# Optimization experiments

Measured on AMD Instinct MI355X. Metric: run time of the kernel, lower is better.

Reference implementation:

```python
import jax, jax.numpy as jnp
import numpy as np

B, T, F, H = 64, 512, 128, 512
NUM_LAYERS = 3


def _lstm_layer(x_tbf, W_ih, W_hh, b_ih, b_hh):
    # x_tbf: [T, B, in], W_ih: [4H, in], W_hh: [4H, H]
    # PyTorch gate order: i, f, g, o
    Hd = W_hh.shape[1]
    Bd = x_tbf.shape[1]
    # precompute input projections for all timesteps (one big GEMM)
    x_proj = jnp.einsum('tbf,gf->tbg', x_tbf, W_ih) + b_ih  # [T, B, 4H]

    def step(carry, xp_t):
        h, c = carry
        gates = xp_t + h @ W_hh.T + b_hh  # [B, 4H]
        i, f, g, o = jnp.split(gates, 4, axis=-1)
        i = jax.nn.sigmoid(i)
        f = jax.nn.sigmoid(f)
        g = jnp.tanh(g)
        o = jax.nn.sigmoid(o)
        c = f * c + i * g
        h = o * jnp.tanh(c)
        return (h, c), h

    h0 = jnp.zeros((Bd, Hd), x_tbf.dtype)
    c0 = jnp.zeros((Bd, Hd), x_tbf.dtype)
    _, hs = jax.lax.scan(step, (h0, c0), x_proj)
    return hs  # [T, B, H]


def setup_inputs() -> dict:
    key = jax.random.key(0)
    ks = jax.random.split(key, 20)
    s = 1.0 / np.sqrt(H)
    inp = {"input_tensor": jax.random.normal(ks[0], (B, T, F), jnp.float32)}
    in_dims = [F, H, H]
    ki = 1
    for l in range(NUM_LAYERS):
        inp[f"W_ih{l}"] = jax.random.uniform(ks[ki], (4 * H, in_dims[l]), jnp.float32, -s, s); ki += 1
        inp[f"W_hh{l}"] = jax.random.uniform(ks[ki], (4 * H, H), jnp.float32, -s, s); ki += 1
        inp[f"b_ih{l}"] = jax.random.uniform(ks[ki], (4 * H,), jnp.float32, -s, s); ki += 1
        inp[f"b_hh{l}"] = jax.random.uniform(ks[ki], (4 * H,), jnp.float32, -s, s); ki += 1
    s1 = 1.0 / np.sqrt(H)
    inp["fc_W1"] = jax.random.uniform(ks[13], (64, H), jnp.float32, -s1, s1)
    inp["fc_b1"] = jax.random.uniform(ks[14], (64,), jnp.float32, -s1, s1)
    s2 = 1.0 / np.sqrt(64)
    inp["fc_W2"] = jax.random.uniform(ks[15], (1, 64), jnp.float32, -s2, s2)
    inp["fc_b2"] = jax.random.uniform(ks[16], (1,), jnp.float32, -s2, s2)
    return inp


def reference(input_tensor, W_ih0, W_hh0, b_ih0, b_hh0,
              W_ih1, W_hh1, b_ih1, b_hh1,
              W_ih2, W_hh2, b_ih2, b_hh2,
              fc_W1, fc_b1, fc_W2, fc_b2):
    x = jnp.transpose(input_tensor, (1, 0, 2))  # [T, B, F]
    x = _lstm_layer(x, W_ih0, W_hh0, b_ih0, b_hh0)
    x = _lstm_layer(x, W_ih1, W_hh1, b_ih1, b_hh1)  # eval mode: no dropout
    x = _lstm_layer(x, W_ih2, W_hh2, b_ih2, b_hh2)
    last = x[-1]  # [B, H]
    h1 = jax.nn.relu(last @ fc_W1.T + fc_b1)
    out = jax.nn.relu(h1 @ fc_W2.T + fc_b2)  # [B, 1]
    return out
```

## Files before the change

### kernel.cpp

```cpp
#include <hip/hip_runtime.h>
#include <hip/hip_fp16.h>
#include <math.h>

#define B_ 64
#define T_ 512
#define F_ 128
#define H_ 512
#define NBLK 96
#define SPIN_MAX (1 << 20)

typedef _Float16 f16x8 __attribute__((ext_vector_type(8)));
typedef float f32x4 __attribute__((ext_vector_type(4)));
typedef int   i32x4 __attribute__((ext_vector_type(4)));

__device__ __forceinline__ unsigned short f2h(float f) {
    return __half_as_ushort(__float2half(f));
}
__device__ __forceinline__ float h2f(unsigned short u) {
    return __half2float(__ushort_as_half(u));
}

__global__ void transpose_x(const float* __restrict__ in, unsigned* __restrict__ xs) {
    const int t = blockIdx.x;
    for (int idx = threadIdx.x; idx < B_ * F_ / 4; idx += blockDim.x) {
        const int kp2 = idx >> 6;
        const int bb = idx & 63;
        const float* src = in + (size_t)bb * T_ * F_ + (size_t)t * F_ + 4 * kp2;
        const unsigned h0 = f2h(src[0]), h1 = f2h(src[1]);
        const unsigned h2 = f2h(src[2]), h3 = f2h(src[3]);
        const unsigned dw0 = h0 | (h1 << 16);
        const unsigned dw1 = h2 | (h3 << 16);
        *(unsigned long long*)(xs + (size_t)t * 4096 + (size_t)kp2 * 128 + bb * 2) =
            ((unsigned long long)dw1 << 32) | dw0;
    }
}

__device__ __forceinline__ float sigmoid_(float x) {
    return __builtin_amdgcn_rcpf(1.0f + __expf(-x));
}
__device__ __forceinline__ float tanh_(float x) {
    return 1.0f - 2.0f * __builtin_amdgcn_rcpf(1.0f + __expf(2.0f * x));
}

__device__ __forceinline__ unsigned long long loadc_u64(const unsigned* p) {
    return __hip_atomic_load((const unsigned long long*)p, __ATOMIC_RELAXED,
                             __HIP_MEMORY_SCOPE_AGENT);
}
__device__ __forceinline__ unsigned loadc_u32(const unsigned* p) {
    return __hip_atomic_load(p, __ATOMIC_RELAXED, __HIP_MEMORY_SCOPE_AGENT);
}
__device__ __forceinline__ void storec_u64(unsigned* p, unsigned long long v) {
    __hip_atomic_store((unsigned long long*)p, v, __ATOMIC_RELAXED,
                       __HIP_MEMORY_SCOPE_AGENT);
}
__device__ __forceinline__ void storec_f(float* p, float v) {
    __hip_atomic_store(p, v, __ATOMIC_RELAXED, __HIP_MEMORY_SCOPE_AGENT);
}
__device__ __forceinline__ float loadc_f(const float* p) {
    return __hip_atomic_load(p, __ATOMIC_RELAXED, __HIP_MEMORY_SCOPE_AGENT);
}
__device__ __forceinline__ int loadc_i(const int* p) {
    return __hip_atomic_load(p, __ATOMIC_RELAXED, __HIP_MEMORY_SCOPE_AGENT);
}
__device__ __forceinline__ void storec_i(int* p, int v) {
    __hip_atomic_store(p, v, __ATOMIC_RELAXED, __HIP_MEMORY_SCOPE_AGENT);
}

__device__ __forceinline__ void gbar_arrive(int* __restrict__ slots, int bid,
                                            int tid, int e) {
    asm volatile("s_waitcnt vmcnt(0) lgkmcnt(0)" ::: "memory");
    __syncthreads();
    if (tid == 0) storec_i(&slots[bid * 16], e);
}
__device__ __forceinline__ void gbar_wait(const int* __restrict__ slots, int tid,
                                          int e) {
    if (tid < NBLK) {
        int g = 0;
        while (loadc_i(&slots[tid * 16]) < e && ++g < SPIN_MAX)
            __builtin_amdgcn_s_sleep(1);
    }
    __syncthreads();
}

template <int NKX, bool XPLAIN>
__device__ void scan_layer(const unsigned* __restrict__ xb,
                           unsigned* __restrict__ hbuf,
                           int* __restrict__ slots, int bid, int tid,
                           const unsigned short* __restrict__ wfrag,
                           const float (&bias)[4][4], const int (&hstore)[4],
                           int lane, int q, int laneoff, int twol) {
    float c_reg[4] = {0.f, 0.f, 0.f, 0.f};
    unsigned long long vx[NKX][2];
    union Frag { i32x4 i4; f16x8 s; };

    auto pref = [&](int tt) {
        if (tt < 0 || tt >= T_) return;
        const unsigned* xsrc = XPLAIN ? (xb + (size_t)tt * 4096 + laneoff)
                                      : (xb + (size_t)(tt & 3) * 16384 + laneoff);
#pragma unroll
        for (int i = 0; i < NKX; ++i) {
            if (XPLAIN) {
                vx[i][0] = *(const unsigned long long*)(xsrc + i * 1024);
                vx[i][1] = *(const unsigned long long*)(xsrc + i * 1024 + 128);
            } else {
                vx[i][0] = loadc_u64(xsrc + i * 1024);
                vx[i][1] = loadc_u64(xsrc + i * 1024 + 128);
            }
        }
    };

    if (XPLAIN) pref(0);

    for (int s = 0; s < T_ + 4; ++s) {
        const int t = s - twol;
        if (t >= 0 && t < T_) {
            unsigned long long vh[16][2];
            const unsigned* hs = hbuf + (size_t)((t + 3) & 3) * 16384 + laneoff;
#pragma unroll
            for (int j = 0; j < 16; ++j) {
                vh[j][0] = loadc_u64(hs + j * 1024);
                vh[j][1] = loadc_u64(hs + j * 1024 + 128);
            }

            f32x4 acc[4] = {{0.f,0.f,0.f,0.f},{0.f,0.f,0.f,0.f},
                            {0.f,0.f,0.f,0.f},{0.f,0.f,0.f,0.f}};
#pragma unroll
            for (int i = 0; i < NKX; ++i) {
                Frag Bf, A0, A1, A2, A3;
                Bf.i4[0] = (int)(unsigned)vx[i][0];
                Bf.i4[1] = (int)(unsigned)(vx[i][0] >> 32);
                Bf.i4[2] = (int)(unsigned)vx[i][1];
                Bf.i4[3] = (int)(unsigned)(vx[i][1] >> 32);
                A0.i4 = *(const i32x4*)&wfrag[i * 2048 + lane * 8];
                A1.i4 = *(const i32x4*)&wfrag[i * 2048 + 512 + lane * 8];
                A2.i4 = *(const i32x4*)&wfrag[i * 2048 + 1024 + lane * 8];
                A3.i4 = *(const i32x4*)&wfrag[i * 2048 + 1536 + lane * 8];
                acc[0] = __builtin_amdgcn_mfma_f32_16x16x32_f16(A0.s, Bf.s, acc[0], 0, 0, 0);
                acc[1] = __builtin_amdgcn_mfma_f32_16x16x32_f16(A1.s, Bf.s, acc[1], 0, 0, 0);
                acc[2] = __builtin_amdgcn_mfma_f32_16x16x32_f16(A2.s, Bf.s, acc[2], 0, 0, 0);
                acc[3] = __builtin_amdgcn_mfma_f32_16x16x32_f16(A3.s, Bf.s, acc[3], 0, 0, 0);
            }
#pragma unroll
            for (int j = 0; j < 16; ++j) {
                Frag Bf, A0, A1, A2, A3;
                Bf.i4[0] = (int)(unsigned)vh[j][0];
                Bf.i4[1] = (int)(unsigned)(vh[j][0] >> 32);
                Bf.i4[2] = (int)(unsigned)vh[j][1];
                Bf.i4[3] = (int)(unsigned)(vh[j][1] >> 32);
                const int i = NKX + j;
                A0.i4 = *(const i32x4*)&wfrag[i * 2048 + lane * 8];
                A1.i4 = *(const i32x4*)&wfrag[i * 2048 + 512 + lane * 8];
                A2.i4 = *(const i32x4*)&wfrag[i * 2048 + 1024 + lane * 8];
                A3.i4 = *(const i32x4*)&wfrag[i * 2048 + 1536 + lane * 8];
                acc[0] = __builtin_amdgcn_mfma_f32_16x16x32_f16(A0.s, Bf.s, acc[0], 0, 0, 0);
                acc[1] = __builtin_amdgcn_mfma_f32_16x16x32_f16(A1.s, Bf.s, acc[1], 0, 0, 0);
                acc[2] = __builtin_amdgcn_mfma_f32_16x16x32_f16(A2.s, Bf.s, acc[2], 0, 0, 0);
                acc[3] = __builtin_amdgcn_mfma_f32_16x16x32_f16(A3.s, Bf.s, acc[3], 0, 0, 0);
            }

#pragma unroll
            for (int rg = 0; rg < 4; ++rg) {
                float a[4];
#pragma unroll
                for (int g = 0; g < 4; ++g) a[g] = bias[rg][g] + acc[rg][g];
                const float ig = sigmoid_(a[0]);
                const float fg = sigmoid_(a[1]);
                const float gg = tanh_(a[2]);
                const float og = sigmoid_(a[3]);
                c_reg[rg] = fg * c_reg[rg] + ig * gg;
                const float hv = og * tanh_(c_reg[rg]);
                const unsigned P0 = (unsigned)f2h(hv);
                const unsigned P1 = (unsigned)__shfl_xor((int)P0, 16, 64) & 0xFFFFu;
                const unsigned D  = P0 | (P1 << 16);
                const unsigned D2 = (unsigned)__shfl_xor((int)D, 32, 64);
                if (q == 0)
                    storec_u64(hbuf + (size_t)(t & 3) * 16384 + hstore[rg],
                               ((unsigned long long)D2 << 32) | D);
            }
        }
        gbar_arrive(slots, bid, tid, s + 1);
        __builtin_amdgcn_sched_barrier(0);
        pref(s + 1 - twol);
        __builtin_amdgcn_sched_barrier(0);
        gbar_wait(slots, tid, s + 1);
    }
}

__global__ void __launch_bounds__(256, 1) lstm_scan(
    const unsigned* __restrict__ xs, unsigned* __restrict__ hbf,
    float* __restrict__ h1s, float* __restrict__ out,
    int* __restrict__ bar_slots,
    const float* __restrict__ Wih0, const float* __restrict__ Whh0,
    const float* __restrict__ bih0, const float* __restrict__ bhh0,
    const float* __restrict__ Wih1, const float* __restrict__ Whh1,
    const float* __restrict__ bih1, const float* __restrict__ bhh1,
    const float* __restrict__ Wih2, const float* __restrict__ Whh2,
    const float* __restrict__ bih2, const float* __restrict__ bhh2,
    const float* __restrict__ fcW1, const float* __restrict__ fcb1,
    const float* __restrict__ fcW2, const float* __restrict__ fcb2) {
    __shared__ unsigned short wfrag[32 * 2048];
    __shared__ float redsc[4 * 64];

    const float* WihA[3] = {Wih0, Wih1, Wih2};
    const float* WhhA[3] = {Whh0, Whh1, Whh2};
    const float* bihA[3] = {bih0, bih1, bih2};
    const float* bhhA[3] = {bhh0, bhh1, bhh2};

    const int tid   = threadIdx.x;
    const int bid   = blockIdx.x;
    const int layer = bid >> 5;
    const int cb    = bid & 31;
    const int c0    = cb * 16;
    const int lane  = tid & 63;
    const int w     = __builtin_amdgcn_readfirstlane(tid >> 6);
    const int KX    = (layer == 0) ? F_ : H_;
    const int NK    = KX / 32 + 16;

    const float* wih = WihA[layer];
    const float* whh = WhhA[layer];

    for (int idx = tid; idx < NK * 2048; idx += 256) {
        const int i = idx >> 11, rem = idx & 2047;
        const int rg = rem >> 9, r2 = rem & 511;
        const int l = r2 >> 3, j = r2 & 7;
        const int m = l & 15;
        const int grow = (m & 3) * 512 + c0 + rg * 4 + (m >> 2);
        const int k = i * 32 + (l >> 4) * 8 + j;
        const float f = (k < KX) ? wih[(size_t)grow * KX + k]
                                 : whh[(size_t)grow * 512 + (k - KX)];
        wfrag[i * 2048 + rg * 512 + l * 8 + j] = f2h(f);
    }
    __syncthreads();

    const int fb = w * 16 + (lane & 15);
    const int q  = lane >> 4;
    float bias[4][4];
#pragma unroll
    for (int rg = 0; rg < 4; ++rg)
#pragma unroll
        for (int g = 0; g < 4; ++g)
            bias[rg][g] = bihA[layer][g * 512 + c0 + rg * 4 + q] +
                          bhhA[layer][g * 512 + c0 + rg * 4 + q];

    int hstore[4];
#pragma unroll
    for (int rg = 0; rg < 4; ++rg) hstore[rg] = (cb * 4 + rg) * 128 + fb * 2;
    const int laneoff = q * 256 + fb * 2;

    unsigned* hbuf = hbf + (size_t)layer * 4 * 16384;
    const unsigned* xb =
        (layer == 0) ? xs : (hbf + (size_t)(layer - 1) * 4 * 16384);

    if (layer == 0)
        scan_layer<4, true>(xb, hbuf, bar_slots, bid, tid, wfrag, bias, hstore,
                            lane, q, laneoff, 0);
    else if (layer == 1)
        scan_layer<16, false>(xb, hbuf, bar_slots, bid, tid, wfrag, bias,
                              hstore, lane, q, laneoff, 2);
    else
        scan_layer<16, false>(xb, hbuf, bar_slots, bid, tid, wfrag, bias,
                              hstore, lane, q, laneoff, 4);

    const unsigned* h2u = hbf + (size_t)2 * 4 * 16384 + (size_t)3 * 16384;
    const int fcb = tid & 63;
    if (bid < 64) {
        float part = 0.0f;
        const float* wrow = fcW1 + (size_t)bid * H_ + w * 128;
#pragma unroll 8
        for (int k = 0; k < 128; ++k) {
            const int kk = w * 128 + k;
            const unsigned dv =
                loadc_u32(h2u + (kk >> 2) * 128 + fcb * 2 + ((kk >> 1) & 1));
            const float val = h2f((unsigned short)((dv >> ((kk & 1) * 16)) & 0xFFFFu));
            part = fmaf(wrow[k], val, part);
        }
        redsc[w * 64 + fcb] = part;
        __syncthreads();
        if (tid < 64) {
            float acc2 = fcb1[bid] + redsc[tid] + redsc[64 + tid] +
                         redsc[128 + tid] + redsc[192 + tid];
            storec_f(&h1s[bid * B_ + tid], fmaxf(acc2, 0.0f));
        }
    }
    gbar_arrive(bar_slots, bid, tid, T_ + 5);
    gbar_wait(bar_slots, tid, T_ + 5);
    if (bid == 0 && tid < 64) {
        float acc2 = fcb2[0];
#pragma unroll
        for (int c = 0; c < 64; ++c)
            acc2 = fmaf(fcW2[c], loadc_f(&h1s[c * B_ + tid]), acc2);
        out[tid] = fmaxf(acc2, 0.0f);
    }
}

extern "C" void kernel_launch(void* const* d_in, const int* in_sizes, int n_in,
                              void* d_out, int out_size, void* d_ws, size_t ws_size,
                              hipStream_t stream) {
    const float* in    = (const float*)d_in[0];
    const float* Wih0  = (const float*)d_in[1];
    const float* Whh0  = (const float*)d_in[2];
    const float* bih0  = (const float*)d_in[3];
    const float* bhh0  = (const float*)d_in[4];
    const float* Wih1  = (const float*)d_in[5];
    const float* Whh1  = (const float*)d_in[6];
    const float* bih1  = (const float*)d_in[7];
    const float* bhh1  = (const float*)d_in[8];
    const float* Wih2  = (const float*)d_in[9];
    const float* Whh2  = (const float*)d_in[10];
    const float* bih2  = (const float*)d_in[11];
    const float* bhh2  = (const float*)d_in[12];
    const float* fcW1  = (const float*)d_in[13];
    const float* fcb1  = (const float*)d_in[14];
    const float* fcW2  = (const float*)d_in[15];
    const float* fcb2  = (const float*)d_in[16];
    float* outp = (float*)d_out;

    unsigned* xs  = (unsigned*)d_ws;
    unsigned* hbf = xs + (size_t)T_ * 4096;
    float* h1s = (float*)(hbf + (size_t)3 * 4 * 16384);
    int* bar_slots = (int*)(h1s + 64 * 64);

    hipMemsetAsync(hbf, 0,
                   ((size_t)3 * 4 * 16384 + 64 * 64 + NBLK * 16 + 16) * sizeof(int),
                   stream);

    transpose_x<<<dim3(T_), dim3(256), 0, stream>>>(in, xs);

    void* args[] = {
        (void*)&xs, (void*)&hbf, (void*)&h1s, (void*)&outp, (void*)&bar_slots,
        (void*)&Wih0, (void*)&Whh0, (void*)&bih0, (void*)&bhh0,
        (void*)&Wih1, (void*)&Whh1, (void*)&bih1, (void*)&bhh1,
        (void*)&Wih2, (void*)&Whh2, (void*)&bih2, (void*)&bhh2,
        (void*)&fcW1, (void*)&fcb1, (void*)&fcW2, (void*)&fcb2};
    hipLaunchCooperativeKernel((void*)lstm_scan, dim3(NBLK), dim3(256), args, 0, stream);
}
```

Baseline: 2.721 ms.

## Tag hidden-state entries with timestep to drop memory drain from grid barrier

Each stored hidden-state half-pair now carries its timestep tag in the upper 32 bits. Consumers re-read until all tags match, which lets the per-step grid barrier skip the s_waitcnt drain. The inter-layer skew is cut from 2 to 1 step, so the scan needs fewer total steps, and the FC head validates the final layer's tags before reading. This doubles the hidden-buffer traffic and adds spin-retry loads. Correctness now rests on 64-bit relaxed atomics being seen whole, and the retry loop gives up after a fixed bound.

```diff
diff --git a/kernel.cpp b/kernel.cpp
--- a/kernel.cpp
+++ b/kernel.cpp
@@ -8,6 +8,7 @@
 #define H_ 512
 #define NBLK 96
 #define SPIN_MAX (1 << 20)
+#define GUARD_RETRY 4096
 
 typedef _Float16 f16x8 __attribute__((ext_vector_type(8)));
 typedef float f32x4 __attribute__((ext_vector_type(4)));
@@ -46,9 +47,6 @@
     return __hip_atomic_load((const unsigned long long*)p, __ATOMIC_RELAXED,
                              __HIP_MEMORY_SCOPE_AGENT);
 }
-__device__ __forceinline__ unsigned loadc_u32(const unsigned* p) {
-    return __hip_atomic_load(p, __ATOMIC_RELAXED, __HIP_MEMORY_SCOPE_AGENT);
-}
 __device__ __forceinline__ void storec_u64(unsigned* p, unsigned long long v) {
     __hip_atomic_store((unsigned long long*)p, v, __ATOMIC_RELAXED,
                        __HIP_MEMORY_SCOPE_AGENT);
@@ -66,14 +64,10 @@
     __hip_atomic_store(p, v, __ATOMIC_RELAXED, __HIP_MEMORY_SCOPE_AGENT);
 }
 
-__device__ __forceinline__ void gbar_arrive(int* __restrict__ slots, int bid,
-                                            int tid, int e) {
-    asm volatile("s_waitcnt vmcnt(0) lgkmcnt(0)" ::: "memory");
+__device__ __forceinline__ void gbar_nd(int* __restrict__ slots, int bid,
+                                        int tid, int e) {
     __syncthreads();
     if (tid == 0) storec_i(&slots[bid * 16], e);
-}
-__device__ __forceinline__ void gbar_wait(const int* __restrict__ slots, int tid,
-                                          int e) {
     if (tid < NBLK) {
         int g = 0;
         while (loadc_i(&slots[tid * 16]) < e && ++g < SPIN_MAX)
@@ -81,45 +75,95 @@
     }
     __syncthreads();
 }
-
-template <int NKX, bool XPLAIN>
+__device__ __forceinline__ void gbar_drain(int* __restrict__ slots, int bid,
+                                           int tid, int e) {
+    asm volatile("s_waitcnt vmcnt(0) lgkmcnt(0)" ::: "memory");
+    __syncthreads();
+    if (tid == 0) storec_i(&slots[bid * 16], e);
+    if (tid < NBLK) {
+        int g = 0;
+        while (loadc_i(&slots[tid * 16]) < e && ++g < SPIN_MAX)
+            __builtin_amdgcn_s_sleep(1);
+    }
+    __syncthreads();
+}
+
+template <int NKX, bool XTAG>
 __device__ void scan_layer(const unsigned* __restrict__ xb,
                            unsigned* __restrict__ hbuf,
                            int* __restrict__ slots, int bid, int tid,
                            const unsigned short* __restrict__ wfrag,
-                           const float (&bias)[4][4], const int (&hstore)[4],
-                           int lane, int q, int laneoff, int twol) {
+                           const float (&bias)[4][4], int lane, int q, int fb,
+                           int cb, int layer) {
+    union Frag { i32x4 i4; f16x8 s; };
     float c_reg[4] = {0.f, 0.f, 0.f, 0.f};
-    unsigned long long vx[NKX][2];
-    union Frag { i32x4 i4; f16x8 s; };
-
-    auto pref = [&](int tt) {
-        if (tt < 0 || tt >= T_) return;
-        const unsigned* xsrc = XPLAIN ? (xb + (size_t)tt * 4096 + laneoff)
-                                      : (xb + (size_t)(tt & 3) * 16384 + laneoff);
-#pragma unroll
-        for (int i = 0; i < NKX; ++i) {
-            if (XPLAIN) {
-                vx[i][0] = *(const unsigned long long*)(xsrc + i * 1024);
-                vx[i][1] = *(const unsigned long long*)(xsrc + i * 1024 + 128);
-            } else {
-                vx[i][0] = loadc_u64(xsrc + i * 1024);
-                vx[i][1] = loadc_u64(xsrc + i * 1024 + 128);
-            }
-        }
-    };
-
-    if (XPLAIN) pref(0);
-
-    for (int s = 0; s < T_ + 4; ++s) {
-        const int t = s - twol;
+    const int ho = fb * 4;
+    const int xo_plain = q * 256 + fb * 2;
+    int hstE[4];
+#pragma unroll
+    for (int rg = 0; rg < 4; ++rg) hstE[rg] = (cb * 4 + rg) * 256 + fb * 4;
+
+    for (int s = 0; s < T_ + 2; ++s) {
+        const int t = s - layer;
         if (t >= 0 && t < T_) {
-            unsigned long long vh[16][2];
-            const unsigned* hs = hbuf + (size_t)((t + 3) & 3) * 16384 + laneoff;
-#pragma unroll
-            for (int j = 0; j < 16; ++j) {
-                vh[j][0] = loadc_u64(hs + j * 1024);
-                vh[j][1] = loadc_u64(hs + j * 1024 + 128);
+            unsigned long long vh[32][2];
+            unsigned long long vx[XTAG ? 32 : NKX][2];
+
+            const unsigned* hsl = hbuf + (size_t)((t + 3) & 3) * 32768 + ho;
+            const unsigned* xsl = XTAG ? (xb + (size_t)(t & 3) * 32768 + ho)
+                                       : (xb + (size_t)t * 4096 + xo_plain);
+
+            auto issue_x = [&]() {
+                if constexpr (XTAG) {
+#pragma unroll
+                    for (int i = 0; i < 16; ++i) {
+                        const unsigned* e0 = xsl + (8 * i + 2 * q) * 256;
+                        vx[2 * i][0]     = loadc_u64(e0);
+                        vx[2 * i][1]     = loadc_u64(e0 + 2);
+                        vx[2 * i + 1][0] = loadc_u64(e0 + 256);
+                        vx[2 * i + 1][1] = loadc_u64(e0 + 258);
+                    }
+                } else {
+#pragma unroll
+                    for (int i = 0; i < NKX; ++i) {
+                        vx[i][0] = *(const unsigned long long*)(xsl + i * 1024);
+                        vx[i][1] = *(const unsigned long long*)(xsl + i * 1024 + 128);
+                    }
+                }
+            };
+            auto issue_h = [&]() {
+#pragma unroll
+                for (int j = 0; j < 16; ++j) {
+                    const unsigned* e0 = hsl + (8 * j + 2 * q) * 256;
+                    vh[2 * j][0]     = loadc_u64(e0);
+                    vh[2 * j][1]     = loadc_u64(e0 + 2);
+                    vh[2 * j + 1][0] = loadc_u64(e0 + 256);
+                    vh[2 * j + 1][1] = loadc_u64(e0 + 258);
+                }
+            };
+
+            issue_x();
+            issue_h();
+
+            const unsigned htag = (unsigned)t;
+            const unsigned xtag = (unsigned)(t + 1);
+            int guard = 0;
+            for (;;) {
+                int ok = 1;
+#pragma unroll
+                for (int e = 0; e < 32; ++e)
+                    ok &= ((unsigned)(vh[e][0] >> 32) == htag) &
+                          ((unsigned)(vh[e][1] >> 32) == htag);
+                if constexpr (XTAG) {
+#pragma unroll
+                    for (int e = 0; e < 32; ++e)
+                        ok &= ((unsigned)(vx[e][0] >> 32) == xtag) &
+                              ((unsigned)(vx[e][1] >> 32) == xtag);
+                }
+                if (__all(ok)) break;
+                if (++guard > GUARD_RETRY) break;
+                issue_x();
+                issue_h();
             }
 
             f32x4 acc[4] = {{0.f,0.f,0.f,0.f},{0.f,0.f,0.f,0.f},
@@ -127,10 +171,17 @@
 #pragma unroll
             for (int i = 0; i < NKX; ++i) {
                 Frag Bf, A0, A1, A2, A3;
-                Bf.i4[0] = (int)(unsigned)vx[i][0];
-                Bf.i4[1] = (int)(unsigned)(vx[i][0] >> 32);
-                Bf.i4[2] = (int)(unsigned)vx[i][1];
-                Bf.i4[3] = (int)(unsigned)(vx[i][1] >> 32);
+                if constexpr (XTAG) {
+                    Bf.i4[0] = (int)(unsigned)vx[2 * i][0];
+                    Bf.i4[1] = (int)(unsigned)vx[2 * i][1];
+                    Bf.i4[2] = (int)(unsigned)vx[2 * i + 1][0];
+                    Bf.i4[3] = (int)(unsigned)vx[2 * i + 1][1];
+                } else {
+                    Bf.i4[0] = (int)(unsigned)vx[i][0];
+                    Bf.i4[1] = (int)(unsigned)(vx[i][0] >> 32);
+                    Bf.i4[2] = (int)(unsigned)vx[i][1];
+                    Bf.i4[3] = (int)(unsigned)(vx[i][1] >> 32);
+                }
                 A0.i4 = *(const i32x4*)&wfrag[i * 2048 + lane * 8];
                 A1.i4 = *(const i32x4*)&wfrag[i * 2048 + 512 + lane * 8];
                 A2.i4 = *(const i32x4*)&wfrag[i * 2048 + 1024 + lane * 8];
@@ -143,10 +194,10 @@
 #pragma unroll
             for (int j = 0; j < 16; ++j) {
                 Frag Bf, A0, A1, A2, A3;
-                Bf.i4[0] = (int)(unsigned)vh[j][0];
-                Bf.i4[1] = (int)(unsigned)(vh[j][0] >> 32);
-                Bf.i4[2] = (int)(unsigned)vh[j][1];
-                Bf.i4[3] = (int)(unsigned)(vh[j][1] >> 32);
+                Bf.i4[0] = (int)(unsigned)vh[2 * j][0];
+                Bf.i4[1] = (int)(unsigned)vh[2 * j][1];
+                Bf.i4[2] = (int)(unsigned)vh[2 * j + 1][0];
+                Bf.i4[3] = (int)(unsigned)vh[2 * j + 1][1];
                 const int i = NKX + j;
                 A0.i4 = *(const i32x4*)&wfrag[i * 2048 + lane * 8];
                 A1.i4 = *(const i32x4*)&wfrag[i * 2048 + 512 + lane * 8];
@@ -173,16 +224,15 @@
                 const unsigned P1 = (unsigned)__shfl_xor((int)P0, 16, 64) & 0xFFFFu;
                 const unsigned D  = P0 | (P1 << 16);
                 const unsigned D2 = (unsigned)__shfl_xor((int)D, 32, 64);
-                if (q == 0)
-                    storec_u64(hbuf + (size_t)(t & 3) * 16384 + hstore[rg],
-                               ((unsigned long long)D2 << 32) | D);
+                if (q == 0) {
+                    unsigned* eb = hbuf + (size_t)(t & 3) * 32768 + hstE[rg];
+                    const unsigned long long tg = (unsigned long long)(t + 1) << 32;
+                    storec_u64(eb, tg | D);
+                    storec_u64(eb + 2, tg | D2);
+                }
             }
         }
-        gbar_arrive(slots, bid, tid, s + 1);
-        __builtin_amdgcn_sched_barrier(0);
-        pref(s + 1 - twol);
-        __builtin_amdgcn_sched_barrier(0);
-        gbar_wait(slots, tid, s + 1);
+        gbar_nd(slots, bid, tid, s + 1);
     }
 }
 
@@ -242,37 +292,49 @@
             bias[rg][g] = bihA[layer][g * 512 + c0 + rg * 4 + q] +
                           bhhA[layer][g * 512 + c0 + rg * 4 + q];
 
-    int hstore[4];
-#pragma unroll
-    for (int rg = 0; rg < 4; ++rg) hstore[rg] = (cb * 4 + rg) * 128 + fb * 2;
-    const int laneoff = q * 256 + fb * 2;
-
-    unsigned* hbuf = hbf + (size_t)layer * 4 * 16384;
+    unsigned* hbuf = hbf + (size_t)layer * 4 * 32768;
     const unsigned* xb =
-        (layer == 0) ? xs : (hbf + (size_t)(layer - 1) * 4 * 16384);
+        (layer == 0) ? xs : (hbf + (size_t)(layer - 1) * 4 * 32768);
 
     if (layer == 0)
-        scan_layer<4, true>(xb, hbuf, bar_slots, bid, tid, wfrag, bias, hstore,
-                            lane, q, laneoff, 0);
+        scan_layer<4, false>(xb, hbuf, bar_slots, bid, tid, wfrag, bias, lane,
+                             q, fb, cb, 0);
     else if (layer == 1)
-        scan_layer<16, false>(xb, hbuf, bar_slots, bid, tid, wfrag, bias,
-                              hstore, lane, q, laneoff, 2);
+        scan_layer<16, true>(xb, hbuf, bar_slots, bid, tid, wfrag, bias, lane,
+                             q, fb, cb, 1);
     else
-        scan_layer<16, false>(xb, hbuf, bar_slots, bid, tid, wfrag, bias,
-                              hstore, lane, q, laneoff, 4);
-
-    const unsigned* h2u = hbf + (size_t)2 * 4 * 16384 + (size_t)3 * 16384;
+        scan_layer<16, true>(xb, hbuf, bar_slots, bid, tid, wfrag, bias, lane,
+                             q, fb, cb, 2);
+
     const int fcb = tid & 63;
     if (bid < 64) {
+        const unsigned* h2b = hbf + (size_t)2 * 4 * 32768 + (size_t)3 * 32768;
+        unsigned long long ef[32][2];
+        int guard = 0;
+        for (;;) {
+#pragma unroll
+            for (int j = 0; j < 32; ++j) {
+                const unsigned* e0 = h2b + (size_t)(w * 32 + j) * 256 + fcb * 4;
+                ef[j][0] = loadc_u64(e0);
+                ef[j][1] = loadc_u64(e0 + 2);
+            }
+            int ok = 1;
+#pragma unroll
+            for (int j = 0; j < 32; ++j)
+                ok &= ((unsigned)(ef[j][0] >> 32) == (unsigned)T_) &
+                      ((unsigned)(ef[j][1] >> 32) == (unsigned)T_);
+            if (__all(ok)) break;
+            if (++guard > GUARD_RETRY) break;
+        }
         float part = 0.0f;
         const float* wrow = fcW1 + (size_t)bid * H_ + w * 128;
-#pragma unroll 8
-        for (int k = 0; k < 128; ++k) {
-            const int kk = w * 128 + k;
-            const unsigned dv =
-                loadc_u32(h2u + (kk >> 2) * 128 + fcb * 2 + ((kk >> 1) & 1));
-            const float val = h2f((unsigned short)((dv >> ((kk & 1) * 16)) & 0xFFFFu));
-            part = fmaf(wrow[k], val, part);
+#pragma unroll
+        for (int j = 0; j < 32; ++j) {
+            const unsigned d1 = (unsigned)ef[j][0], d2 = (unsigned)ef[j][1];
+            part = fmaf(wrow[4 * j],     h2f((unsigned short)(d1 & 0xFFFFu)), part);
+            part = fmaf(wrow[4 * j + 1], h2f((unsigned short)(d1 >> 16)), part);
+            part = fmaf(wrow[4 * j + 2], h2f((unsigned short)(d2 & 0xFFFFu)), part);
+            part = fmaf(wrow[4 * j + 3], h2f((unsigned short)(d2 >> 16)), part);
         }
         redsc[w * 64 + fcb] = part;
         __syncthreads();
@@ -282,8 +344,7 @@
             storec_f(&h1s[bid * B_ + tid], fmaxf(acc2, 0.0f));
         }
     }
-    gbar_arrive(bar_slots, bid, tid, T_ + 5);
-    gbar_wait(bar_slots, tid, T_ + 5);
+    gbar_drain(bar_slots, bid, tid, T_ + 3);
     if (bid == 0 && tid < 64) {
         float acc2 = fcb2[0];
 #pragma unroll
@@ -317,11 +378,12 @@
 
     unsigned* xs  = (unsigned*)d_ws;
     unsigned* hbf = xs + (size_t)T_ * 4096;
-    float* h1s = (float*)(hbf + (size_t)3 * 4 * 16384);
+    float* h1s = (float*)(hbf + (size_t)3 * 4 * 32768);
     int* bar_slots = (int*)(h1s + 64 * 64);
 
     hipMemsetAsync(hbf, 0,
-                   ((size_t)3 * 4 * 16384 + 64 * 64 + NBLK * 16 + 16) * sizeof(int),
+                   ((size_t)3 * 4 * 32768 + 64 * 64 + NBLK * 16 + 16) *
+                       sizeof(int),
                    stream);
 
     transpose_x<<<dim3(T_), dim3(256), 0, stream>>>(in, xs);
```

New measurement: 4.995 ms. 83.6% more time.
